# Optimization experiments

Measured on AMD Instinct MI355X. Metric: run time of the kernel, lower is better.

## Reference

```python
import jax, jax.numpy as jnp
import numpy as np

N_NODES = 100000
N_GRAPHS = 256


def gcn_conv(x, W, b, src, dst, n_nodes):
    # PyG GCNConv: h = x @ W; out_i = sum_{(j->i)} norm_e * h_j + norm_ii * h_i + b
    # with self-loops added and norm = deg^{-1/2}[src] * deg^{-1/2}[dst],
    # deg counting self-loops.
    h = x @ W                                            # [N, H]
    ones = jnp.ones(src.shape[0], dtype=x.dtype)
    deg = jax.ops.segment_sum(ones, dst, num_segments=n_nodes) + 1.0  # +1 self-loop
    dis = jax.lax.rsqrt(deg)                             # deg >= 1 always
    norm = dis[src] * dis[dst]                           # [E]
    msg = h[src] * norm[:, None]                         # [E, H] gather + scale
    agg = jax.ops.segment_sum(msg, dst, num_segments=n_nodes)         # scatter-add
    self_loop = h * (dis * dis)[:, None]                 # norm_ii = dis_i^2
    return agg + self_loop + b


def setup_inputs() -> dict:
    key = jax.random.key(0)
    ks = jax.random.split(key, 8)
    C_IN, H = 64, 64
    E = 1600000
    x = jax.random.normal(ks[0], (N_NODES, C_IN), dtype=jnp.float32)
    edge_index = jax.random.randint(ks[1], (2, E), 0, N_NODES, dtype=jnp.int64)
    batch = jnp.sort(jax.random.randint(ks[2], (N_NODES,), 0, N_GRAPHS, dtype=jnp.int64))
    s = 0.1
    W1 = jax.random.normal(ks[3], (C_IN, H), dtype=jnp.float32) * s
    W2 = jax.random.normal(ks[4], (H, H), dtype=jnp.float32) * s
    W3 = jax.random.normal(ks[5], (H, H), dtype=jnp.float32) * s
    Wl = jax.random.normal(ks[6], (H, 1), dtype=jnp.float32) * s
    b1 = jnp.zeros((H,), jnp.float32)
    b2 = jnp.zeros((H,), jnp.float32)
    b3 = jnp.zeros((H,), jnp.float32)
    bl = jnp.zeros((1,), jnp.float32)
    return {"x": x, "edge_index": edge_index, "batch": batch,
            "W1": W1, "b1": b1, "W2": W2, "b2": b2, "W3": W3, "b3": b3,
            "Wl": Wl, "bl": bl}


def reference(x, edge_index, batch, W1, b1, W2, b2, W3, b3, Wl, bl):
    src, dst = edge_index[0], edge_index[1]
    n = x.shape[0]
    h = jax.nn.relu(gcn_conv(x, W1, b1, src, dst, n))
    h = jax.nn.relu(gcn_conv(h, W2, b2, src, dst, n))
    h = gcn_conv(h, W3, b3, src, dst, n)
    # global_mean_pool over graph ids
    sums = jax.ops.segment_sum(h, batch, num_segments=N_GRAPHS)        # [G, H]
    cnt = jax.ops.segment_sum(jnp.ones((n,), h.dtype), batch, num_segments=N_GRAPHS)
    pooled = sums / jnp.maximum(cnt, 1.0)[:, None]
    # dropout p=0.5 is identity at inference (training=False)
    return pooled @ Wl + bl                                            # [G, 1]
```

## Files before the change

kernel.cpp:

```cpp
#include <hip/hip_runtime.h>

#define NGRAPHS 256
#define GBUCKET 256
#define CAP 8192
#define BUCKET_BLOCKS 512
#define MAXE 16

typedef unsigned long long u64;


__global__ __launch_bounds__(256) void k_bucket(const int* __restrict__ src,
                                                const int* __restrict__ dst,
                                                int E, int N,
                                                int* __restrict__ bcur,
                                                u64* __restrict__ bpair) {
    __shared__ int hist[GBUCKET], base[GBUCKET], cur[GBUCKET];
    int t = threadIdx.x;
    int chunk = (E + gridDim.x - 1) / gridDim.x;
    int s0 = blockIdx.x * chunk;
    int s1 = s0 + chunk; if (s1 > E) s1 = E;
    if (s0 >= E) return;
    for (int i = t; i < GBUCKET; i += 256) hist[i] = 0;
    __syncthreads();

    int dcache[MAXE], scache[MAXE], bcache[MAXE];
#pragma unroll
    for (int u = 0; u < MAXE; ++u) {
        int e = s0 + t + u * 256;
        bool ok = e < s1;
        int d = ok ? __builtin_nontemporal_load(&dst[e]) : -1;
        int s = ok ? __builtin_nontemporal_load(&src[e]) : 0;
        int bkt = ok ? (int)(((long long)d * GBUCKET) / N) : -1;
        dcache[u] = d; scache[u] = s; bcache[u] = bkt;
        if (ok) atomicAdd(&hist[bkt], 1);
    }
    __syncthreads();
    for (int i = t; i < GBUCKET; i += 256) {
        base[i] = atomicAdd(&bcur[i], hist[i]);
        cur[i] = 0;
    }
    __syncthreads();
#pragma unroll
    for (int u = 0; u < MAXE; ++u) {
        int bkt = bcache[u];
        if (bkt >= 0) {
            int off = atomicAdd(&cur[bkt], 1);
            u64 p = ((u64)(unsigned)dcache[u] << 32) | (u64)(unsigned)scache[u];
            __builtin_nontemporal_store(p, &bpair[(size_t)bkt * CAP + base[bkt] + off]);
        }
    }
}


__global__ __launch_bounds__(512) void k_csr(const int* __restrict__ bcur,
                                             const u64* __restrict__ bpair,
                                             int N, int E,
                                             int* __restrict__ row_start,
                                             float* __restrict__ dis,
                                             int* __restrict__ csr_src) {
    __shared__ int cnts[512];
    __shared__ int scanbuf[512];
    __shared__ int cursors[512];
    __shared__ int bb[GBUCKET];
    __shared__ int bbase_s, bcnt_s;
    int g = blockIdx.x;
    int t = threadIdx.x;

    for (int i = t; i < GBUCKET; i += 512) bb[i] = bcur[i];
    cnts[t] = 0;
    __syncthreads();
    if (t == 0) {
        int s = 0;
        for (int k = 0; k < g; ++k) s += bb[k];
        bbase_s = s;
        bcnt_s = bb[g];
    }
    __syncthreads();
    int bbase = bbase_s;
    int cnt   = bcnt_s;

    int lo = (int)(((long long)g * N + GBUCKET - 1) / GBUCKET);
    int hi = (int)(((long long)(g + 1) * N + GBUCKET - 1) / GBUCKET);
    int nn = hi - lo;

    const u64* bp = bpair + (size_t)g * CAP;
    for (int i = t; i < cnt; i += 512) {
        u64 p = __builtin_nontemporal_load(&bp[i]);
        atomicAdd(&cnts[(int)(p >> 32) - lo], 1);
    }
    __syncthreads();

    int v = cnts[t];
    scanbuf[t] = v;
    __syncthreads();
    for (int o = 1; o < 512; o <<= 1) {
        int add = (t >= o) ? scanbuf[t - o] : 0;
        __syncthreads();
        scanbuf[t] += add;
        __syncthreads();
    }
    int excl = scanbuf[t] - v;

    if (t < nn) {
        row_start[lo + t] = bbase + excl;
        dis[lo + t] = rsqrtf((float)v + 1.0f);
    }
    if (g == GBUCKET - 1 && t == 0) row_start[N] = E;
    cursors[t] = excl;
    __syncthreads();

    for (int i = t; i < cnt; i += 512) {
        u64 p = __builtin_nontemporal_load(&bp[i]);
        int d = (int)(p >> 32);
        int s = (int)(p & 0xffffffffu);
        int pos = bbase + atomicAdd(&cursors[d - lo], 1);
        csr_src[pos] = s;
    }
}


__global__ __launch_bounds__(256) void k_gemm64(const float* __restrict__ X,
                                                const float* __restrict__ W,
                                                const float* __restrict__ dis,
                                                float* __restrict__ G, int N) {
    __shared__ float ws[64 * 64];
    __shared__ float xs[64 * 64];
    int t = threadIdx.x;
    int row0 = blockIdx.x * 64;
    int nr = N - row0; if (nr > 64) nr = 64;

    const float4* W4 = (const float4*)W;
    float4* ws4 = (float4*)ws;
    for (int i = t; i < 1024; i += 256) ws4[i] = W4[i];
    const float4* X4 = (const float4*)(X + (size_t)row0 * 64);
    float4* xs4 = (float4*)xs;
    for (int i = t; i < nr * 16; i += 256) xs4[i] = X4[i];
    __syncthreads();

    int col = t & 63;
    int rg  = t >> 6;
    float acc[16];
#pragma unroll
    for (int j = 0; j < 16; ++j) acc[j] = 0.0f;

    for (int k4 = 0; k4 < 16; ++k4) {
        float w0 = ws[(k4 * 4 + 0) * 64 + col];
        float w1 = ws[(k4 * 4 + 1) * 64 + col];
        float w2 = ws[(k4 * 4 + 2) * 64 + col];
        float w3 = ws[(k4 * 4 + 3) * 64 + col];
#pragma unroll
        for (int j = 0; j < 16; ++j) {
            float4 xv = xs4[(rg * 16 + j) * 16 + k4];
            acc[j] = fmaf(xv.x, w0, acc[j]);
            acc[j] = fmaf(xv.y, w1, acc[j]);
            acc[j] = fmaf(xv.z, w2, acc[j]);
            acc[j] = fmaf(xv.w, w3, acc[j]);
        }
    }
#pragma unroll
    for (int j = 0; j < 16; ++j) {
        int r = rg * 16 + j;
        if (r < nr) G[(size_t)(row0 + r) * 64 + col] = acc[j] * dis[row0 + r];
    }
}


template <bool RELU, bool POOL>
__global__ __launch_bounds__(256) void k_agg(const float* __restrict__ g,
                                             const float* __restrict__ dis,
                                             const int* __restrict__ row_start,
                                             const int* __restrict__ csr_src,
                                             const float* __restrict__ b,
                                             float* __restrict__ out, int N,
                                             const float* __restrict__ Wl,
                                             float* __restrict__ hdot) {
    int wave0 = (blockIdx.x * blockDim.x + threadIdx.x) >> 6;
    int nwaves = (gridDim.x * blockDim.x) >> 6;
    int lane = threadIdx.x & 63;
    int sub  = lane >> 4;
    int q    = lane & 15;
    const float4* g4 = (const float4*)g;

    for (int wid = wave0; wid < N; wid += nwaves) {
        int beg = row_start[wid];
        int end = row_start[wid + 1];

        float4 acc;
        if (sub == 0) acc = g4[(size_t)wid * 16 + q];
        else          acc = make_float4(0.f, 0.f, 0.f, 0.f);

        int e = beg;
        for (; e + 8 <= end; e += 8) {
            int sA = csr_src[e + sub];
            int sB = csr_src[e + 4 + sub];
            float4 a = g4[(size_t)sA * 16 + q];
            float4 c = g4[(size_t)sB * 16 + q];
            acc.x += a.x; acc.y += a.y; acc.z += a.z; acc.w += a.w;
            acc.x += c.x; acc.y += c.y; acc.z += c.z; acc.w += c.w;
        }
        if (e + 4 <= end) {
            int sA = csr_src[e + sub];
            float4 a = g4[(size_t)sA * 16 + q];
            acc.x += a.x; acc.y += a.y; acc.z += a.z; acc.w += a.w;
            e += 4;
        }
        int rem = end - e;
        if (sub < rem) {
            int sA = csr_src[e + sub];
            float4 a = g4[(size_t)sA * 16 + q];
            acc.x += a.x; acc.y += a.y; acc.z += a.z; acc.w += a.w;
        }

#pragma unroll
        for (int o = 16; o <= 32; o <<= 1) {
            acc.x += __shfl_xor(acc.x, o);
            acc.y += __shfl_xor(acc.y, o);
            acc.z += __shfl_xor(acc.z, o);
            acc.w += __shfl_xor(acc.w, o);
        }

        if (sub == 0) {
            float d = dis[wid];
            float4 bv = ((const float4*)b)[q];
            float4 v;
            v.x = fmaf(acc.x, d, bv.x);
            v.y = fmaf(acc.y, d, bv.y);
            v.z = fmaf(acc.z, d, bv.z);
            v.w = fmaf(acc.w, d, bv.w);
            if (RELU) {
                v.x = fmaxf(v.x, 0.f); v.y = fmaxf(v.y, 0.f);
                v.z = fmaxf(v.z, 0.f); v.w = fmaxf(v.w, 0.f);
            }
            if (POOL) {
                float4 wl = ((const float4*)Wl)[q];
                float s = v.x * wl.x + v.y * wl.y + v.z * wl.z + v.w * wl.w;
                s += __shfl_xor(s, 1);
                s += __shfl_xor(s, 2);
                s += __shfl_xor(s, 4);
                s += __shfl_xor(s, 8);
                if (q == 0) hdot[wid] = s;
            } else {
                ((float4*)out)[(size_t)wid * 16 + q] = v;
            }
        }
    }
}


__global__ __launch_bounds__(256) void k_poolfin(const float* __restrict__ hdot,
                                                 const int* __restrict__ batch,
                                                 const float* __restrict__ bl,
                                                 float* __restrict__ out, int N) {
    int g = blockIdx.x;
    int lo = 0, hi = N;
    while (lo < hi) { int m = (lo + hi) >> 1; if (batch[m] < g) lo = m + 1; else hi = m; }
    int start = lo;
    hi = N;
    while (lo < hi) { int m = (lo + hi) >> 1; if (batch[m] <= g) lo = m + 1; else hi = m; }
    int end = lo;

    float part = 0.0f;
    for (int i = start + threadIdx.x; i < end; i += 256)
        part += hdot[i];
    for (int o = 32; o; o >>= 1) part += __shfl_down(part, o);
    __shared__ float ps[4];
    int lane = threadIdx.x & 63;
    int wv = threadIdx.x >> 6;
    if (lane == 0) ps[wv] = part;
    __syncthreads();
    if (threadIdx.x == 0) {
        float s = ps[0] + ps[1] + ps[2] + ps[3];
        float cnt = (float)(end - start);
        out[g] = s / fmaxf(cnt, 1.0f) + bl[0];
    }
}


extern "C" void kernel_launch(void* const* d_in, const int* in_sizes, int n_in,
                              void* d_out, int out_size, void* d_ws, size_t ws_size,
                              hipStream_t stream) {
    const float* x     = (const float*)d_in[0];
    const int*   ei    = (const int*)d_in[1];
    const int*   batch = (const int*)d_in[2];
    const float* W1 = (const float*)d_in[3];
    const float* b1 = (const float*)d_in[4];
    const float* W2 = (const float*)d_in[5];
    const float* b2 = (const float*)d_in[6];
    const float* W3 = (const float*)d_in[7];
    const float* b3 = (const float*)d_in[8];
    const float* Wl = (const float*)d_in[9];
    const float* bl = (const float*)d_in[10];
    float* out = (float*)d_out;

    const int N = in_sizes[0] / 64;
    const int E = in_sizes[1] / 2;
    const int* src = ei;
    const int* dst = ei + E;

    char* w = (char*)d_ws;
    auto alloc = [&](size_t bytes) -> void* {
        void* p = (void*)w;
        w += (bytes + 255) & ~(size_t)255;
        return p;
    };
    float* hA        = (float*)alloc((size_t)N * 64 * 4);
    float* hB        = (float*)alloc((size_t)N * 64 * 4);
    int*   csr       = (int*)alloc((size_t)E * 4);
    float* dis       = (float*)alloc((size_t)N * 4);
    int*   row_start = (int*)alloc((size_t)(N + 1) * 4);
    int*   bcur      = (int*)alloc((size_t)GBUCKET * 4);
    float* hdot      = (float*)alloc((size_t)N * 4);

    u64* bpair = (u64*)hA;

    (void)hipMemsetAsync(bcur, 0, (size_t)GBUCKET * 4, stream);

    k_bucket<<<BUCKET_BLOCKS, 256, 0, stream>>>(src, dst, E, N, bcur, bpair);
    k_csr<<<GBUCKET, 512, 0, stream>>>(bcur, bpair, N, E, row_start, dis, csr);

    int gb = (N + 63) / 64;
    int ab = 2048;

    k_gemm64<<<gb, 256, 0, stream>>>(x, W1, dis, hA, N);
    k_agg<true, false><<<ab, 256, 0, stream>>>(hA, dis, row_start, csr, b1, hB, N, Wl, nullptr);
    k_gemm64<<<gb, 256, 0, stream>>>(hB, W2, dis, hA, N);
    k_agg<true, false><<<ab, 256, 0, stream>>>(hA, dis, row_start, csr, b2, hB, N, Wl, nullptr);
    k_gemm64<<<gb, 256, 0, stream>>>(hB, W3, dis, hA, N);
    k_agg<false, true><<<ab, 256, 0, stream>>>(hA, dis, row_start, csr, b3, nullptr, N, Wl, hdot);

    k_poolfin<<<NGRAPHS, 256, 0, stream>>>(hdot, batch, bl, out, N);
}
```

Baseline: 370.6 us.

## Fuse next-layer GEMM into aggregation kernel epilogue

The per-node aggregation kernel now loads the next layer's 64x64 weight into shared memory and, after computing the activated row, multiplies it by the weight using wave shuffles, writing the pre-scaled features for the next layer directly. This removes two standalone GEMM launches and one full write and read of the intermediate node features per layer. In exchange, every wave does a 64-wide matvec per node via shuffles and LDS reads, and each block uses 16 KB of shared memory, which may lower occupancy for the latency-bound gather.

```diff
diff --git a/kernel.cpp b/kernel.cpp
--- a/kernel.cpp
+++ b/kernel.cpp
@@ -165,15 +165,22 @@
 }
 
 
-template <bool RELU, bool POOL>
-__global__ __launch_bounds__(256) void k_agg(const float* __restrict__ g,
-                                             const float* __restrict__ dis,
-                                             const int* __restrict__ row_start,
-                                             const int* __restrict__ csr_src,
-                                             const float* __restrict__ b,
-                                             float* __restrict__ out, int N,
-                                             const float* __restrict__ Wl,
-                                             float* __restrict__ hdot) {
+template <bool POOL>
+__global__ __launch_bounds__(256) void k_fused(const float* __restrict__ g,
+                                               const float* __restrict__ dis,
+                                               const int* __restrict__ row_start,
+                                               const int* __restrict__ csr_src,
+                                               const float* __restrict__ b,
+                                               const float* __restrict__ Wn,
+                                               float* __restrict__ out, int N) {
+    __shared__ float ws[64 * 64];
+    if (!POOL) {
+        const float4* W4 = (const float4*)Wn;
+        float4* ws4 = (float4*)ws;
+        for (int i = threadIdx.x; i < 1024; i += 256) ws4[i] = W4[i];
+        __syncthreads();
+    }
+
     int wave0 = (blockIdx.x * blockDim.x + threadIdx.x) >> 6;
     int nwaves = (gridDim.x * blockDim.x) >> 6;
     int lane = threadIdx.x & 63;
@@ -219,28 +226,39 @@
             acc.w += __shfl_xor(acc.w, o);
         }
 
-        if (sub == 0) {
-            float d = dis[wid];
-            float4 bv = ((const float4*)b)[q];
-            float4 v;
-            v.x = fmaf(acc.x, d, bv.x);
-            v.y = fmaf(acc.y, d, bv.y);
-            v.z = fmaf(acc.z, d, bv.z);
-            v.w = fmaf(acc.w, d, bv.w);
-            if (RELU) {
-                v.x = fmaxf(v.x, 0.f); v.y = fmaxf(v.y, 0.f);
-                v.z = fmaxf(v.z, 0.f); v.w = fmaxf(v.w, 0.f);
+        float d = dis[wid];
+        float4 bv = ((const float4*)b)[q];
+        float4 v;
+        v.x = fmaf(acc.x, d, bv.x);
+        v.y = fmaf(acc.y, d, bv.y);
+        v.z = fmaf(acc.z, d, bv.z);
+        v.w = fmaf(acc.w, d, bv.w);
+
+        if (!POOL) {
+            v.x = fmaxf(v.x, 0.f); v.y = fmaxf(v.y, 0.f);
+            v.z = fmaxf(v.z, 0.f); v.w = fmaxf(v.w, 0.f);
+            float u = 0.0f;
+#pragma unroll
+            for (int kq = 0; kq < 16; ++kq) {
+                float vx = __shfl(v.x, kq);
+                float vy = __shfl(v.y, kq);
+                float vz = __shfl(v.z, kq);
+                float vw = __shfl(v.w, kq);
+                u = fmaf(vx, ws[(4 * kq + 0) * 64 + lane], u);
+                u = fmaf(vy, ws[(4 * kq + 1) * 64 + lane], u);
+                u = fmaf(vz, ws[(4 * kq + 2) * 64 + lane], u);
+                u = fmaf(vw, ws[(4 * kq + 3) * 64 + lane], u);
             }
-            if (POOL) {
-                float4 wl = ((const float4*)Wl)[q];
+            out[(size_t)wid * 64 + lane] = u * d;
+        } else {
+            if (sub == 0) {
+                float4 wl = ((const float4*)Wn)[q];
                 float s = v.x * wl.x + v.y * wl.y + v.z * wl.z + v.w * wl.w;
                 s += __shfl_xor(s, 1);
                 s += __shfl_xor(s, 2);
                 s += __shfl_xor(s, 4);
                 s += __shfl_xor(s, 8);
-                if (q == 0) hdot[wid] = s;
-            } else {
-                ((float4*)out)[(size_t)wid * 16 + q] = v;
+                if (q == 0) out[wid] = s;
             }
         }
     }
@@ -322,11 +340,9 @@
     int ab = 2048;
 
     k_gemm64<<<gb, 256, 0, stream>>>(x, W1, dis, hA, N);
-    k_agg<true, false><<<ab, 256, 0, stream>>>(hA, dis, row_start, csr, b1, hB, N, Wl, nullptr);
-    k_gemm64<<<gb, 256, 0, stream>>>(hB, W2, dis, hA, N);
-    k_agg<true, false><<<ab, 256, 0, stream>>>(hA, dis, row_start, csr, b2, hB, N, Wl, nullptr);
-    k_gemm64<<<gb, 256, 0, stream>>>(hB, W3, dis, hA, N);
-    k_agg<false, true><<<ab, 256, 0, stream>>>(hA, dis, row_start, csr, b3, nullptr, N, Wl, hdot);
+    k_fused<false><<<ab, 256, 0, stream>>>(hA, dis, row_start, csr, b1, W2, hB, N);
+    k_fused<false><<<ab, 256, 0, stream>>>(hB, dis, row_start, csr, b2, W3, hA, N);
+    k_fused<true><<<ab, 256, 0, stream>>>(hA, dis, row_start, csr, b3, Wl, hdot, N);
 
     k_poolfin<<<NGRAPHS, 256, 0, stream>>>(hdot, batch, bl, out, N);
 }
```

Result: slower. 385.7 us (+4.1%).

## Replace LDS-tiled GEMM with register-resident weights and wave-per-row loop

Applied to the files above, without the earlier changes.

The shared-memory tiled 64x64 GEMM is replaced by a grid-stride kernel. Each lane keeps one column of W in 64 registers, and each wave computes one row at a time, reading that row through wave-uniform scalar loads. This removes LDS staging and barriers and uses a fixed grid of 2048 blocks. The trade-offs are 64 extra VGPRs per thread, which can lower occupancy, and per-row scalar loads from global memory with no reuse across rows.

```diff
diff --git a/kernel.cpp b/kernel.cpp
--- a/kernel.cpp
+++ b/kernel.cpp
@@ -119,48 +119,31 @@
 }
 
 
-__global__ __launch_bounds__(256) void k_gemm64(const float* __restrict__ X,
-                                                const float* __restrict__ W,
-                                                const float* __restrict__ dis,
-                                                float* __restrict__ G, int N) {
-    __shared__ float ws[64 * 64];
-    __shared__ float xs[64 * 64];
-    int t = threadIdx.x;
-    int row0 = blockIdx.x * 64;
-    int nr = N - row0; if (nr > 64) nr = 64;
-
-    const float4* W4 = (const float4*)W;
-    float4* ws4 = (float4*)ws;
-    for (int i = t; i < 1024; i += 256) ws4[i] = W4[i];
-    const float4* X4 = (const float4*)(X + (size_t)row0 * 64);
-    float4* xs4 = (float4*)xs;
-    for (int i = t; i < nr * 16; i += 256) xs4[i] = X4[i];
-    __syncthreads();
-
-    int col = t & 63;
-    int rg  = t >> 6;
-    float acc[16];
-#pragma unroll
-    for (int j = 0; j < 16; ++j) acc[j] = 0.0f;
-
-    for (int k4 = 0; k4 < 16; ++k4) {
-        float w0 = ws[(k4 * 4 + 0) * 64 + col];
-        float w1 = ws[(k4 * 4 + 1) * 64 + col];
-        float w2 = ws[(k4 * 4 + 2) * 64 + col];
-        float w3 = ws[(k4 * 4 + 3) * 64 + col];
-#pragma unroll
-        for (int j = 0; j < 16; ++j) {
-            float4 xv = xs4[(rg * 16 + j) * 16 + k4];
-            acc[j] = fmaf(xv.x, w0, acc[j]);
-            acc[j] = fmaf(xv.y, w1, acc[j]);
-            acc[j] = fmaf(xv.z, w2, acc[j]);
-            acc[j] = fmaf(xv.w, w3, acc[j]);
-        }
-    }
-#pragma unroll
-    for (int j = 0; j < 16; ++j) {
-        int r = rg * 16 + j;
-        if (r < nr) G[(size_t)(row0 + r) * 64 + col] = acc[j] * dis[row0 + r];
+__global__ __launch_bounds__(256) void k_gemm_reg(const float* __restrict__ X,
+                                                  const float* __restrict__ W,
+                                                  const float* __restrict__ dis,
+                                                  float* __restrict__ G, int N) {
+    int lane = threadIdx.x & 63;
+    int wid = (blockIdx.x * blockDim.x + threadIdx.x) >> 6;
+    int nw = (gridDim.x * blockDim.x) >> 6;
+
+    float wreg[64];
+#pragma unroll
+    for (int k = 0; k < 64; ++k) wreg[k] = W[k * 64 + lane];
+
+    for (int r = wid; r < N; r += nw) {
+        int ru = __builtin_amdgcn_readfirstlane(r);
+        const float* xr = X + (size_t)ru * 64;
+        float a0 = 0.f, a1 = 0.f, a2 = 0.f, a3 = 0.f;
+#pragma unroll
+        for (int k = 0; k < 64; k += 4) {
+            a0 = fmaf(xr[k + 0], wreg[k + 0], a0);
+            a1 = fmaf(xr[k + 1], wreg[k + 1], a1);
+            a2 = fmaf(xr[k + 2], wreg[k + 2], a2);
+            a3 = fmaf(xr[k + 3], wreg[k + 3], a3);
+        }
+        float a = (a0 + a1) + (a2 + a3);
+        G[(size_t)ru * 64 + lane] = a * dis[ru];
     }
 }
 
@@ -318,14 +301,14 @@
     k_bucket<<<BUCKET_BLOCKS, 256, 0, stream>>>(src, dst, E, N, bcur, bpair);
     k_csr<<<GBUCKET, 512, 0, stream>>>(bcur, bpair, N, E, row_start, dis, csr);
 
-    int gb = (N + 63) / 64;
+    int gmb = 2048;
     int ab = 2048;
 
-    k_gemm64<<<gb, 256, 0, stream>>>(x, W1, dis, hA, N);
+    k_gemm_reg<<<gmb, 256, 0, stream>>>(x, W1, dis, hA, N);
     k_agg<true, false><<<ab, 256, 0, stream>>>(hA, dis, row_start, csr, b1, hB, N, Wl, nullptr);
-    k_gemm64<<<gb, 256, 0, stream>>>(hB, W2, dis, hA, N);
+    k_gemm_reg<<<gmb, 256, 0, stream>>>(hB, W2, dis, hA, N);
     k_agg<true, false><<<ab, 256, 0, stream>>>(hA, dis, row_start, csr, b2, hB, N, Wl, nullptr);
-    k_gemm64<<<gb, 256, 0, stream>>>(hB, W3, dis, hA, N);
+    k_gemm_reg<<<gmb, 256, 0, stream>>>(hB, W3, dis, hA, N);
     k_agg<false, true><<<ab, 256, 0, stream>>>(hA, dis, row_start, csr, b3, nullptr, N, Wl, hdot);
 
     k_poolfin<<<NGRAPHS, 256, 0, stream>>>(hdot, batch, bl, out, N);
```

New measurement: 368.8 us. No clear change (-0.5%).
